# Performance work log

Measured on AMD Instinct MI355X. Metric: run time of the kernel, lower is better.

The kernel has to match this reference:

```python
import jax, jax.numpy as jnp
import numpy as np

N = 100000   # nodes
E = 1600000  # edges
H = 128      # hidden_channels
G = 2        # group
D = H // G   # per-group channels
L = 2        # num_layers
T = 112      # num_tasks
MSG_EPS = 1e-7


def _ln(x, g, b):
    mu = jnp.mean(x, axis=-1, keepdims=True)
    var = jnp.var(x, axis=-1, keepdims=True)
    return (x - mu) * jax.lax.rsqrt(var + 1e-5) * g + b


def setup_inputs() -> dict:
    key = jax.random.key(0)
    ks = jax.random.split(key, 12)
    s8, s16, sH, sD = 1/np.sqrt(8), 1/np.sqrt(16), 1/np.sqrt(H), 1/np.sqrt(D)
    inp = {}
    inp["x"] = jax.random.uniform(ks[0], (N, 8), jnp.float32)
    inp["node_index"] = jax.random.randint(ks[1], (N,), 0, N)
    inp["edge_index"] = jax.random.randint(ks[2], (2, E), 0, N)
    inp["edge_attr"] = jax.random.uniform(ks[3], (E, 8), jnp.float32)
    inp["node_features"] = jax.random.normal(ks[4], (N, 8), jnp.float32)
    inp["W_oh"] = jax.random.normal(ks[5], (8, 8)) * s8
    inp["b_oh"] = jnp.zeros((8,))
    inp["W_ne"] = jax.random.normal(ks[6], (16, H)) * s16
    inp["b_ne"] = jnp.zeros((H,))
    inp["W_ee"] = jax.random.normal(ks[7], (8, H)) * s8
    inp["b_ee"] = jnp.zeros((H,))
    inp["ln_g"] = jnp.ones((L, G, D))
    inp["ln_b"] = jnp.zeros((L, G, D))
    inp["We"] = jax.random.normal(ks[8], (L, G, H, D)) * sH   # GENConv edge encoder per Fm
    inp["be"] = jnp.zeros((L, G, D))
    inp["Wm"] = jax.random.normal(ks[9], (L, G, D, D)) * sD   # GENConv 1-layer MLP
    inp["bm"] = jnp.zeros((L, G, D))
    inp["last_g"] = jnp.ones((H,))
    inp["last_b"] = jnp.zeros((H,))
    inp["Wp"] = jax.random.normal(ks[10], (H, T)) * sH
    inp["bp"] = jnp.zeros((T,))
    return inp


def _gen_block(y_in, src, dst, ee, g, b, We_, be_, Wm_, bm_):
    # GENBlock (res+ pre-activation): norm -> relu -> GENConv(softmax aggr, t=1)
    h = jax.nn.relu(_ln(y_in, g, b))                       # [N,D]
    msg = jax.nn.relu(h[src] + ee @ We_ + be_) + MSG_EPS   # [E,D]
    mx = jax.lax.stop_gradient(jax.ops.segment_max(msg, dst, num_segments=N))
    mx = jnp.where(jnp.isfinite(mx), mx, 0.0)
    ex = jnp.exp(msg - mx[dst])
    den = jax.ops.segment_sum(ex, dst, num_segments=N)
    w = ex / (den[dst] + 1e-16)                            # scatter_softmax weights
    agg = jax.ops.segment_sum(msg * w, dst, num_segments=N)  # [N,D]
    return (h + agg) @ Wm_ + bm_


def reference(x, node_index, edge_index, edge_attr, node_features, W_oh, b_oh, W_ne, b_ne, W_ee, b_ee, ln_g, ln_b, We, be, Wm, bm, last_g, last_b, Wp, bp):
    nf1 = node_features[node_index]                        # [N,8]
    nf2 = x @ W_oh + b_oh                                  # one-hot encoder [N,8]
    h = jnp.concatenate([nf1, nf2], axis=1) @ W_ne + b_ne  # [N,H]
    ee = edge_attr @ W_ee + b_ee                           # [E,H]; cat of G copies chunks back to identical [E,H]
    src, dst = edge_index[0], edge_index[1]
    for l in range(L):
        # GroupAdditiveCoupling (group=2): y_i = x_i + F_i(y_{i-1})
        x1, x2 = jnp.split(h, G, axis=-1)
        y1 = x1 + _gen_block(x2, src, dst, ee, ln_g[l, 0], ln_b[l, 0], We[l, 0], be[l, 0], Wm[l, 0], bm[l, 0])
        y2 = x2 + _gen_block(y1, src, dst, ee, ln_g[l, 1], ln_b[l, 1], We[l, 1], be[l, 1], Wm[l, 1], bm[l, 1])
        h = jnp.concatenate([y1, y2], axis=-1)
    h = jax.nn.relu(_ln(h, last_g, last_b))
    return h @ Wp + bp
```

## Files before the change

### kernel.cpp

```cpp
#include <hip/hip_runtime.h>

constexpr int N_NODES = 100000;
constexpr int N_EDGES = 1600000;
constexpr int T_OUT = 112;

constexpr int SCAN_CHUNK = 1024;
constexpr int SCAN_BLOCKS = (N_NODES + SCAN_CHUNK - 1) / SCAN_CHUNK;

typedef _Float16 h2v __attribute__((ext_vector_type(2)));
typedef _Float16 half4 __attribute__((ext_vector_type(4)));
typedef _Float16 half8 __attribute__((ext_vector_type(8)));
typedef float f32x4 __attribute__((ext_vector_type(4)));
typedef int i4v __attribute__((ext_vector_type(4)));
typedef float f4v __attribute__((ext_vector_type(4)));

__device__ __forceinline__ float dot2h(h2v a, h2v b, float c) {
#if __has_builtin(__builtin_amdgcn_fdot2)
    return __builtin_amdgcn_fdot2(a, b, c, false);
#else
    return fmaf((float)a.x, (float)b.x, fmaf((float)a.y, (float)b.y, c));
#endif
}
__device__ __forceinline__ int pk2(float a, float b) {
    auto v = __builtin_amdgcn_cvt_pkrtz(a, b);
    return __builtin_bit_cast(int, v);
}
__device__ __forceinline__ h2v b2h(int x) { return __builtin_bit_cast(h2v, x); }
__device__ __forceinline__ unsigned short f2h(float f) {
    return __builtin_bit_cast(unsigned short, (_Float16)f);
}
__device__ __forceinline__ float h2f(unsigned short u) {
    return (float)__builtin_bit_cast(_Float16, u);
}

__global__ void wcomb_kernel(const float* __restrict__ W_ee,
                             const float* __restrict__ b_ee,
                             const float* __restrict__ We,
                             const float* __restrict__ be,
                             int* __restrict__ Wc_h2,
                             float* __restrict__ bcomb) {
    int lg = blockIdx.x;
    int d = threadIdx.x;
    const float* We_ = We + (size_t)lg * 128 * 64;
    float acc[9];
#pragma unroll
    for (int k = 0; k < 9; ++k) acc[k] = 0.f;
    for (int c = 0; c < 128; ++c) {
        float wv = We_[c * 64 + d];
#pragma unroll
        for (int k = 0; k < 8; ++k) acc[k] += W_ee[k * 128 + c] * wv;
        acc[8] += b_ee[c] * wv;
    }
#pragma unroll
    for (int j = 0; j < 4; ++j)
        Wc_h2[lg * 256 + j * 64 + d] = pk2(acc[2 * j], acc[2 * j + 1]);
    bcomb[lg * 64 + d] = acc[8] + be[lg * 64 + d];
}

__global__ void wp_pack_kernel(const float* __restrict__ Wp, int* __restrict__ wpfrag) {
    int tm = blockIdx.x;
    int tile = tm >> 2, m = tm & 3;
    int lane = threadIdx.x;
    int g = lane >> 4, r = lane & 15;
    int t = tile * 16 + r;
    int o[4];
#pragma unroll
    for (int p = 0; p < 4; ++p) {
        int j0 = 2 * p, j1 = 2 * p + 1;
        int k0 = m * 32 + (j0 >> 2) * 16 + g * 4 + (j0 & 3);
        int k1 = m * 32 + (j1 >> 2) * 16 + g * 4 + (j1 & 3);
        o[p] = pk2(Wp[k0 * 112 + t], Wp[k1 * 112 + t]);
    }
    int4 o4; o4.x = o[0]; o4.y = o[1]; o4.z = o[2]; o4.w = o[3];
    *(int4*)(wpfrag + ((size_t)tm * 64 + lane) * 4) = o4;
}

__global__ void wm_pack_kernel(const float* __restrict__ Wm, int* __restrict__ wmfrag) {
    int b = blockIdx.x;
    int lg = b >> 3, tm = b & 7;
    int tile = tm >> 1, m = tm & 1;
    int lane = threadIdx.x;
    int g = lane >> 4, r = lane & 15;
    const float* W = Wm + (size_t)lg * 4096;
    int col = tile * 16 + r;
    int o[4];
#pragma unroll
    for (int p = 0; p < 4; ++p) {
        int j0 = 2 * p, j1 = 2 * p + 1;
        int k0 = m * 32 + (j0 >> 2) * 16 + g * 4 + (j0 & 3);
        int k1 = m * 32 + (j1 >> 2) * 16 + g * 4 + (j1 & 3);
        o[p] = pk2(W[k0 * 64 + col], W[k1 * 64 + col]);
    }
    int4 o4; o4.x = o[0]; o4.y = o[1]; o4.z = o[2]; o4.w = o[3];
    *(int4*)(wmfrag + ((size_t)b * 64 + lane) * 4) = o4;
}

__global__ __launch_bounds__(256) void encoder_kernel(
    const float* __restrict__ x, const int* __restrict__ node_index,
    const float* __restrict__ node_features,
    const float* __restrict__ W_oh, const float* __restrict__ b_oh,
    const float* __restrict__ W_ne, const float* __restrict__ b_ne,
    float* __restrict__ A, float* __restrict__ B) {
    int tid = threadIdx.x;
    int w = tid >> 6, d = tid & 63;
    int n = blockIdx.x * 4 + w;

    float xf[8];
    const float* xr = x + (size_t)n * 8;
#pragma unroll
    for (int j = 0; j < 8; ++j) xf[j] = xr[j];

    float nf[16];
    int ni = node_index[n];
    const float* nfr = node_features + (size_t)ni * 8;
#pragma unroll
    for (int k = 0; k < 8; ++k) nf[k] = nfr[k];
#pragma unroll
    for (int k = 0; k < 8; ++k) {
        float acc = b_oh[k];
#pragma unroll
        for (int j = 0; j < 8; ++j) acc += xf[j] * W_oh[j * 8 + k];
        nf[8 + k] = acc;
    }
    float hA = b_ne[d], hB = b_ne[64 + d];
#pragma unroll
    for (int k = 0; k < 16; ++k) {
        hA += nf[k] * W_ne[k * 128 + d];
        hB += nf[k] * W_ne[k * 128 + 64 + d];
    }
    A[(size_t)n * 64 + d] = hA;
    B[(size_t)n * 64 + d] = hB;
}

__global__ void hist_kernel(const int* __restrict__ edge_index,
                            int* __restrict__ deg, int* __restrict__ rank) {
    int e = blockIdx.x * 256 + threadIdx.x;
    if (e < N_EDGES) rank[e] = atomicAdd(&deg[edge_index[N_EDGES + e]], 1);
}

__global__ __launch_bounds__(256) void block_sum_kernel(const int* __restrict__ deg,
                                                        int* __restrict__ blocksum) {
    __shared__ int s_w[4];
    int t = threadIdx.x;
    int base = blockIdx.x * SCAN_CHUNK + t * 4;
    int s = 0;
    if (base + 3 < N_NODES) {
        int4 v = *(const int4*)(deg + base);
        s = v.x + v.y + v.z + v.w;
    } else {
        for (int j = 0; j < 4; ++j)
            if (base + j < N_NODES) s += deg[base + j];
    }
#pragma unroll
    for (int o = 32; o >= 1; o >>= 1) s += __shfl_xor(s, o, 64);
    if ((t & 63) == 0) s_w[t >> 6] = s;
    __syncthreads();
    if (t == 0) blocksum[blockIdx.x] = s_w[0] + s_w[1] + s_w[2] + s_w[3];
}

__global__ __launch_bounds__(64) void scan_sums_kernel(const int* __restrict__ blocksum,
                                                       int* __restrict__ blockoff,
                                                       int* __restrict__ rowptr) {
    int t = threadIdx.x;
    int i0 = 2 * t, i1 = 2 * t + 1;
    int v0 = (i0 < SCAN_BLOCKS) ? blocksum[i0] : 0;
    int v1 = (i1 < SCAN_BLOCKS) ? blocksum[i1] : 0;
    int s = v0 + v1;
    int incl = s;
#pragma unroll
    for (int o = 1; o < 64; o <<= 1) {
        int u = __shfl_up(incl, o, 64);
        if (t >= o) incl += u;
    }
    int excl = incl - s;
    if (i0 < SCAN_BLOCKS) blockoff[i0] = excl;
    if (i1 < SCAN_BLOCKS) blockoff[i1] = excl + v0;
    if (t == 63) rowptr[N_NODES] = incl;
}

__global__ __launch_bounds__(256) void emit_kernel(const int* __restrict__ deg,
                                                   const int* __restrict__ blockoff,
                                                   int* __restrict__ rowptr) {
    __shared__ int s_w[4];
    int t = threadIdx.x;
    int w = t >> 6, lane = t & 63;
    int base = blockIdx.x * SCAN_CHUNK + t * 4;

    int d0 = 0, d1 = 0, d2 = 0, d3 = 0;
    if (base + 3 < N_NODES) {
        int4 v = *(const int4*)(deg + base);
        d0 = v.x; d1 = v.y; d2 = v.z; d3 = v.w;
    } else {
        if (base + 0 < N_NODES) d0 = deg[base + 0];
        if (base + 1 < N_NODES) d1 = deg[base + 1];
        if (base + 2 < N_NODES) d2 = deg[base + 2];
        if (base + 3 < N_NODES) d3 = deg[base + 3];
    }
    int s = d0 + d1 + d2 + d3;
    int incl = s;
#pragma unroll
    for (int o = 1; o < 64; o <<= 1) {
        int u = __shfl_up(incl, o, 64);
        if (lane >= o) incl += u;
    }
    if (lane == 63) s_w[w] = incl;
    __syncthreads();
    int woff = 0;
    for (int j = 0; j < 4; ++j) woff += (j < w) ? s_w[j] : 0;

    int p = blockoff[blockIdx.x] + woff + incl - s;
    int4 r;
    r.x = p;
    r.y = p + d0;
    r.z = p + d0 + d1;
    r.w = p + d0 + d1 + d2;
    if (base + 3 < N_NODES) {
        *(int4*)(rowptr + base) = r;
    } else {
        if (base + 0 < N_NODES) rowptr[base + 0] = r.x;
        if (base + 1 < N_NODES) rowptr[base + 1] = r.y;
        if (base + 2 < N_NODES) rowptr[base + 2] = r.z;
        if (base + 3 < N_NODES) rowptr[base + 3] = r.w;
    }
}

__global__ void scatter_kernel(const int* __restrict__ edge_index,
                               const float* __restrict__ edge_attr,
                               const int* __restrict__ rowptr,
                               const int* __restrict__ rank,
                               int* __restrict__ src_perm,
                               int* __restrict__ ea_h) {
    int e = blockIdx.x * 256 + threadIdx.x;
    if (e >= N_EDGES) return;
    int dn = edge_index[N_EDGES + e];
    int idx = rowptr[dn] + rank[e];
    f4v a = __builtin_nontemporal_load((const f4v*)(edge_attr + (size_t)e * 8));
    f4v b = __builtin_nontemporal_load((const f4v*)(edge_attr + (size_t)e * 8 + 4));
    i4v o;
    o.x = pk2(a.x, a.y);
    o.y = pk2(a.z, a.w);
    o.z = pk2(b.x, b.y);
    o.w = pk2(b.z, b.w);
    __builtin_nontemporal_store(o, (i4v*)(ea_h + (size_t)idx * 4));
    __builtin_nontemporal_store(edge_index[e], src_perm + idx);
}

__global__ __launch_bounds__(256) void ln_relu_kernel(const float* __restrict__ Y,
                                                      const float* __restrict__ g,
                                                      const float* __restrict__ b,
                                                      unsigned short* __restrict__ hl16) {
    int tid = threadIdx.x;
    int w = tid >> 6, d = tid & 63;
    int n = blockIdx.x * 4 + w;
    float y = Y[(size_t)n * 64 + d];
    float s = y, sq = y * y;
#pragma unroll
    for (int offd = 32; offd >= 1; offd >>= 1) {
        s += __shfl_xor(s, offd, 64);
        sq += __shfl_xor(sq, offd, 64);
    }
    float mean = s * (1.f / 64.f);
    float var = sq * (1.f / 64.f) - mean * mean;
    float rs = rsqrtf(var + 1e-5f);
    float h = (y - mean) * rs * g[d] + b[d];
    hl16[(size_t)n * 64 + d] = f2h(fmaxf(h, 0.f));
}

__global__ __launch_bounds__(256) void agg_kernel(
    const unsigned short* __restrict__ hl_in, unsigned short* __restrict__ v16,
    const int* __restrict__ rowptr, const int* __restrict__ src_perm,
    const int* __restrict__ ea_h,
    const int* __restrict__ Wc_h2, const float* __restrict__ bcomb) {
    int tid = threadIdx.x;
    int w = tid >> 6, lane = tid & 63;
    int half = lane >> 5;
    int c = (lane & 31) * 2;
    int n = blockIdx.x * 8 + w * 2 + half;

    h2v wc0[4], wc1[4];
#pragma unroll
    for (int j = 0; j < 4; ++j) {
        wc0[j] = b2h(Wc_h2[j * 64 + c]);
        wc1[j] = b2h(Wc_h2[j * 64 + c + 1]);
    }
    float bc0 = bcomb[c], bc1 = bcomb[c + 1];

    float num0 = 0.f, den0 = 0.f, num1 = 0.f, den1 = 0.f;
    int start = rowptr[n], end = rowptr[n + 1];
    const int4* ea4 = (const int4*)ea_h;

#define EDGE(U, E)                                                        \
    {                                                                     \
        h2v hv = b2h((int)(U));                                           \
        float eW0 = bc0, eW1 = bc1;                                       \
        eW0 = dot2h(b2h(E.x), wc0[0], eW0);                               \
        eW1 = dot2h(b2h(E.x), wc1[0], eW1);                               \
        eW0 = dot2h(b2h(E.y), wc0[1], eW0);                               \
        eW1 = dot2h(b2h(E.y), wc1[1], eW1);                               \
        eW0 = dot2h(b2h(E.z), wc0[2], eW0);                               \
        eW1 = dot2h(b2h(E.z), wc1[2], eW1);                               \
        eW0 = dot2h(b2h(E.w), wc0[3], eW0);                               \
        eW1 = dot2h(b2h(E.w), wc1[3], eW1);                               \
        float m0 = fmaxf((float)hv.x + eW0, 0.f) + 1e-7f;                 \
        float m1 = fmaxf((float)hv.y + eW1, 0.f) + 1e-7f;                 \
        float x0 = __expf(m0), x1 = __expf(m1);                           \
        den0 += x0; num0 += x0 * m0;                                      \
        den1 += x1; num1 += x1 * m1;                                      \
    }

    int i = start;
    for (; i + 4 <= end; i += 4) {
        int s0 = src_perm[i + 0];
        int s1 = src_perm[i + 1];
        int s2 = src_perm[i + 2];
        int s3 = src_perm[i + 3];
        unsigned int u0 = *(const unsigned int*)(hl_in + (size_t)s0 * 64 + c);
        unsigned int u1 = *(const unsigned int*)(hl_in + (size_t)s1 * 64 + c);
        unsigned int u2 = *(const unsigned int*)(hl_in + (size_t)s2 * 64 + c);
        unsigned int u3 = *(const unsigned int*)(hl_in + (size_t)s3 * 64 + c);
        int4 e0 = ea4[i + 0], e1 = ea4[i + 1], e2 = ea4[i + 2], e3 = ea4[i + 3];
        EDGE(u0, e0) EDGE(u1, e1) EDGE(u2, e2) EDGE(u3, e3)
    }
    for (; i < end; ++i) {
        int s0 = src_perm[i];
        unsigned int u0 = *(const unsigned int*)(hl_in + (size_t)s0 * 64 + c);
        int4 e0 = ea4[i];
        EDGE(u0, e0)
    }
#undef EDGE

    float agg0 = num0 / (den0 + 1e-16f);
    float agg1 = num1 / (den1 + 1e-16f);
    unsigned int uself = *(const unsigned int*)(hl_in + (size_t)n * 64 + c);
    h2v sv = b2h((int)uself);
    int vout = pk2((float)sv.x + agg0, (float)sv.y + agg1);
    *(int*)(v16 + (size_t)n * 64 + c) = vout;
}

template <bool PRODUCE_HL>
__global__ __launch_bounds__(256) void epi_kernel(
    const unsigned short* __restrict__ v16, float* __restrict__ Y,
    const int* __restrict__ wmfrag, const float* __restrict__ bm,
    const float* __restrict__ gnext, const float* __restrict__ bnext,
    unsigned short* __restrict__ hl_out) {
    int tid = threadIdx.x;
    int w = tid >> 6, lane = tid & 63;
    int g = lane >> 4, r = lane & 15;
    int nodebase = blockIdx.x * 64 + w * 16;
    if (nodebase >= N_NODES) return;

    const unsigned short* vp = v16 + (size_t)(nodebase + r) * 64;
    half8 af[2];
#pragma unroll
    for (int m = 0; m < 2; ++m) {
        int k0 = m * 32 + g * 4;
        half4 lo = *(const half4*)(vp + k0);
        half4 hi = *(const half4*)(vp + k0 + 16);
        af[m][0] = lo[0]; af[m][1] = lo[1]; af[m][2] = lo[2]; af[m][3] = lo[3];
        af[m][4] = hi[0]; af[m][5] = hi[1]; af[m][6] = hi[2]; af[m][7] = hi[3];
    }

    const int4* wf4 = (const int4*)wmfrag;
    f32x4 acc[4];
#pragma unroll
    for (int tile = 0; tile < 4; ++tile) {
        float bmv = bm[tile * 16 + r];
        acc[tile] = {bmv, bmv, bmv, bmv};
#pragma unroll
        for (int m = 0; m < 2; ++m) {
            int4 bw = wf4[(tile * 2 + m) * 64 + lane];
            half8 bf = __builtin_bit_cast(half8, bw);
            acc[tile] = __builtin_amdgcn_mfma_f32_16x16x32_f16(af[m], bf, acc[tile], 0, 0, 0);
        }
    }

    float yn[4][4];
#pragma unroll
    for (int tile = 0; tile < 4; ++tile) {
#pragma unroll
        for (int q = 0; q < 4; ++q) {
            size_t idx = (size_t)(nodebase + g * 4 + q) * 64 + tile * 16 + r;
            float y = Y[idx] + acc[tile][q];
            yn[tile][q] = y;
            Y[idx] = y;
        }
    }

    if constexpr (PRODUCE_HL) {
        float gnv[4], bnv[4];
#pragma unroll
        for (int tile = 0; tile < 4; ++tile) {
            gnv[tile] = gnext[tile * 16 + r];
            bnv[tile] = bnext[tile * 16 + r];
        }
#pragma unroll
        for (int q = 0; q < 4; ++q) {
            float s = yn[0][q] + yn[1][q] + yn[2][q] + yn[3][q];
            float sq = yn[0][q] * yn[0][q] + yn[1][q] * yn[1][q]
                     + yn[2][q] * yn[2][q] + yn[3][q] * yn[3][q];
            s += __shfl_xor(s, 1, 64);  sq += __shfl_xor(sq, 1, 64);
            s += __shfl_xor(s, 2, 64);  sq += __shfl_xor(sq, 2, 64);
            s += __shfl_xor(s, 4, 64);  sq += __shfl_xor(sq, 4, 64);
            s += __shfl_xor(s, 8, 64);  sq += __shfl_xor(sq, 8, 64);
            float mean = s * (1.f / 64.f);
            float var = sq * (1.f / 64.f) - mean * mean;
            float rs = rsqrtf(var + 1e-5f);
#pragma unroll
            for (int tile = 0; tile < 4; ++tile) {
                float h = (yn[tile][q] - mean) * rs * gnv[tile] + bnv[tile];
                hl_out[(size_t)(nodebase + g * 4 + q) * 64 + tile * 16 + r] =
                    f2h(fmaxf(h, 0.f));
            }
        }
    }
}

__global__ __launch_bounds__(256) void final_kernel(
    const float* __restrict__ A, const float* __restrict__ B,
    const float* __restrict__ lg, const float* __restrict__ lb,
    const int* __restrict__ wpfrag, const float* __restrict__ bp,
    float* __restrict__ out) {
    int tid = threadIdx.x;
    int w = tid >> 6, lane = tid & 63;
    int g = lane >> 4, r = lane & 15;
    int nodebase = blockIdx.x * 64 + w * 16;
    if (nodebase >= N_NODES) return;
    int n = nodebase + r;

    float4 v[8];
    const float4* A4 = (const float4*)(A + (size_t)n * 64);
    const float4* B4 = (const float4*)(B + (size_t)n * 64);
#pragma unroll
    for (int kb = 0; kb < 4; ++kb) v[kb] = A4[kb * 4 + g];
#pragma unroll
    for (int kb = 0; kb < 4; ++kb) v[4 + kb] = B4[kb * 4 + g];

    float s = 0.f, sq = 0.f;
#pragma unroll
    for (int kb = 0; kb < 8; ++kb) {
        s += v[kb].x + v[kb].y + v[kb].z + v[kb].w;
        sq += v[kb].x * v[kb].x + v[kb].y * v[kb].y
            + v[kb].z * v[kb].z + v[kb].w * v[kb].w;
    }
    s += __shfl_xor(s, 16, 64);  sq += __shfl_xor(sq, 16, 64);
    s += __shfl_xor(s, 32, 64);  sq += __shfl_xor(sq, 32, 64);
    float mean = s * (1.f / 128.f);
    float var = sq * (1.f / 128.f) - mean * mean;
    float rs = rsqrtf(var + 1e-5f);

    const float4* lg4 = (const float4*)lg;
    const float4* lb4 = (const float4*)lb;
    half8 afr[4];
#pragma unroll
    for (int kb = 0; kb < 8; ++kb) {
        float4 gv = lg4[kb * 4 + g];
        float4 bv = lb4[kb * 4 + g];
        int m = kb >> 1, e0 = (kb & 1) * 4;
        afr[m][e0 + 0] = (_Float16)fmaxf((v[kb].x - mean) * rs * gv.x + bv.x, 0.f);
        afr[m][e0 + 1] = (_Float16)fmaxf((v[kb].y - mean) * rs * gv.y + bv.y, 0.f);
        afr[m][e0 + 2] = (_Float16)fmaxf((v[kb].z - mean) * rs * gv.z + bv.z, 0.f);
        afr[m][e0 + 3] = (_Float16)fmaxf((v[kb].w - mean) * rs * gv.w + bv.w, 0.f);
    }

    const int4* wf4 = (const int4*)wpfrag;
#pragma unroll
    for (int tile = 0; tile < 7; ++tile) {
        float bias = bp[tile * 16 + r];
        f32x4 acc = {bias, bias, bias, bias};
#pragma unroll
        for (int m = 0; m < 4; ++m) {
            int4 bw = wf4[(tile * 4 + m) * 64 + lane];
            half8 bf = __builtin_bit_cast(half8, bw);
            acc = __builtin_amdgcn_mfma_f32_16x16x32_f16(afr[m], bf, acc, 0, 0, 0);
        }
#pragma unroll
        for (int q = 0; q < 4; ++q) {
            out[(size_t)(nodebase + g * 4 + q) * T_OUT + tile * 16 + r] = acc[q];
        }
    }
}

extern "C" void kernel_launch(void* const* d_in, const int* in_sizes, int n_in,
                              void* d_out, int out_size, void* d_ws, size_t ws_size,
                              hipStream_t stream) {
    const float* x            = (const float*)d_in[0];
    const int* node_index     = (const int*)d_in[1];
    const int* edge_index     = (const int*)d_in[2];
    const float* edge_attr    = (const float*)d_in[3];
    const float* node_features= (const float*)d_in[4];
    const float* W_oh         = (const float*)d_in[5];
    const float* b_oh         = (const float*)d_in[6];
    const float* W_ne         = (const float*)d_in[7];
    const float* b_ne         = (const float*)d_in[8];
    const float* W_ee         = (const float*)d_in[9];
    const float* b_ee         = (const float*)d_in[10];
    const float* ln_g         = (const float*)d_in[11];
    const float* ln_b         = (const float*)d_in[12];
    const float* We           = (const float*)d_in[13];
    const float* be           = (const float*)d_in[14];
    const float* Wm           = (const float*)d_in[15];
    const float* bm           = (const float*)d_in[16];
    const float* last_g       = (const float*)d_in[17];
    const float* last_b       = (const float*)d_in[18];
    const float* Wp           = (const float*)d_in[19];
    const float* bp           = (const float*)d_in[20];
    float* out = (float*)d_out;

    char* ws = (char*)d_ws;
    size_t off = 0;
    auto alloc = [&](size_t bytes) -> void* {
        void* p = ws + off;
        off = (off + bytes + 255) & ~(size_t)255;
        return p;
    };
    float* A          = (float*)alloc((size_t)N_NODES * 64 * 4);
    float* B          = (float*)alloc((size_t)N_NODES * 64 * 4);
    unsigned short* hl = (unsigned short*)alloc((size_t)N_NODES * 64 * 2);
    unsigned short* v16 = (unsigned short*)alloc((size_t)N_NODES * 64 * 2);
    int* deg          = (int*)alloc((size_t)N_NODES * 4);
    int* rowptr       = (int*)alloc((size_t)(N_NODES + 1) * 4);
    int* rank         = (int*)alloc((size_t)N_EDGES * 4);
    int* src_perm     = (int*)alloc((size_t)N_EDGES * 4);
    int* ea_h         = (int*)alloc((size_t)N_EDGES * 4 * 4);
    int* Wc_h2        = (int*)alloc(4 * 256 * 4);
    float* bcomb      = (float*)alloc(4 * 64 * 4);
    int* blocksum     = (int*)alloc((size_t)SCAN_BLOCKS * 4);
    int* blockoff     = (int*)alloc((size_t)SCAN_BLOCKS * 4);
    int* wpfrag       = (int*)alloc((size_t)28 * 64 * 16);
    int* wmfrag       = (int*)alloc((size_t)32 * 64 * 16);
    (void)ws_size; (void)in_sizes; (void)n_in; (void)out_size;

    const int NB_NODE = N_NODES / 4;
    const int NB_EDGE = (N_EDGES + 255) / 256;
    const int NB_AGG  = N_NODES / 8;
    const int NB_EPI  = (N_NODES + 63) / 64;

    (void)hipMemsetAsync(deg, 0, (size_t)N_NODES * 4, stream);
    wcomb_kernel<<<4, 64, 0, stream>>>(W_ee, b_ee, We, be, Wc_h2, bcomb);
    wp_pack_kernel<<<28, 64, 0, stream>>>(Wp, wpfrag);
    wm_pack_kernel<<<32, 64, 0, stream>>>(Wm, wmfrag);
    encoder_kernel<<<NB_NODE, 256, 0, stream>>>(x, node_index, node_features,
                                                W_oh, b_oh, W_ne, b_ne, A, B);
    hist_kernel<<<NB_EDGE, 256, 0, stream>>>(edge_index, deg, rank);
    block_sum_kernel<<<SCAN_BLOCKS, 256, 0, stream>>>(deg, blocksum);
    scan_sums_kernel<<<1, 64, 0, stream>>>(blocksum, blockoff, rowptr);
    emit_kernel<<<SCAN_BLOCKS, 256, 0, stream>>>(deg, blockoff, rowptr);
    scatter_kernel<<<NB_EDGE, 256, 0, stream>>>(edge_index, edge_attr, rowptr,
                                                rank, src_perm, ea_h);

    ln_relu_kernel<<<NB_NODE, 256, 0, stream>>>(B, ln_g, ln_b, hl);

    agg_kernel<<<NB_AGG, 256, 0, stream>>>(hl, v16, rowptr, src_perm, ea_h,
                                           Wc_h2 + 0 * 256, bcomb + 0 * 64);
    epi_kernel<true><<<NB_EPI, 256, 0, stream>>>(
        v16, A, wmfrag + 0 * 8 * 256, bm + 0 * 64,
        ln_g + 1 * 64, ln_b + 1 * 64, hl);
    agg_kernel<<<NB_AGG, 256, 0, stream>>>(hl, v16, rowptr, src_perm, ea_h,
                                           Wc_h2 + 1 * 256, bcomb + 1 * 64);
    epi_kernel<true><<<NB_EPI, 256, 0, stream>>>(
        v16, B, wmfrag + 1 * 8 * 256, bm + 1 * 64,
        ln_g + 2 * 64, ln_b + 2 * 64, hl);
    agg_kernel<<<NB_AGG, 256, 0, stream>>>(hl, v16, rowptr, src_perm, ea_h,
                                           Wc_h2 + 2 * 256, bcomb + 2 * 64);
    epi_kernel<true><<<NB_EPI, 256, 0, stream>>>(
        v16, A, wmfrag + 2 * 8 * 256, bm + 2 * 64,
        ln_g + 3 * 64, ln_b + 3 * 64, hl);
    agg_kernel<<<NB_AGG, 256, 0, stream>>>(hl, v16, rowptr, src_perm, ea_h,
                                           Wc_h2 + 3 * 256, bcomb + 3 * 64);
    epi_kernel<false><<<NB_EPI, 256, 0, stream>>>(
        v16, B, wmfrag + 3 * 8 * 256, bm + 3 * 64,
        nullptr, nullptr, nullptr);

    final_kernel<<<NB_EPI, 256, 0, stream>>>(A, B, last_g, last_b, wpfrag, bp, out);
}
```

Baseline: 608.0 us.

## Two-pass bucketed edge scatter and switch node features from fp16 to fp32

```diff
diff --git a/kernel.cpp b/kernel.cpp
--- a/kernel.cpp
+++ b/kernel.cpp
@@ -7,11 +7,14 @@
 constexpr int SCAN_CHUNK = 1024;
 constexpr int SCAN_BLOCKS = (N_NODES + SCAN_CHUNK - 1) / SCAN_CHUNK;
 
+constexpr int BKT_SHIFT = 9;
+constexpr int NBKT = (N_NODES + 511) / 512;
+constexpr int CHUNK = 4096;
+constexpr int NCHUNK = (N_EDGES + CHUNK - 1) / CHUNK;
+
 typedef _Float16 h2v __attribute__((ext_vector_type(2)));
-typedef _Float16 half4 __attribute__((ext_vector_type(4)));
 typedef _Float16 half8 __attribute__((ext_vector_type(8)));
 typedef float f32x4 __attribute__((ext_vector_type(4)));
-typedef int i4v __attribute__((ext_vector_type(4)));
 typedef float f4v __attribute__((ext_vector_type(4)));
 
 __device__ __forceinline__ float dot2h(h2v a, h2v b, float c) {
@@ -26,12 +29,6 @@
     return __builtin_bit_cast(int, v);
 }
 __device__ __forceinline__ h2v b2h(int x) { return __builtin_bit_cast(h2v, x); }
-__device__ __forceinline__ unsigned short f2h(float f) {
-    return __builtin_bit_cast(unsigned short, (_Float16)f);
-}
-__device__ __forceinline__ float h2f(unsigned short u) {
-    return (float)__builtin_bit_cast(_Float16, u);
-}
 
 __global__ void wcomb_kernel(const float* __restrict__ W_ee,
                              const float* __restrict__ b_ee,
@@ -132,10 +129,25 @@
     B[(size_t)n * 64 + d] = hB;
 }
 
-__global__ void hist_kernel(const int* __restrict__ edge_index,
-                            int* __restrict__ deg, int* __restrict__ rank) {
-    int e = blockIdx.x * 256 + threadIdx.x;
-    if (e < N_EDGES) rank[e] = atomicAdd(&deg[edge_index[N_EDGES + e]], 1);
+__global__ __launch_bounds__(256) void hist_count_kernel(
+    const int* __restrict__ edge_index, int* __restrict__ deg,
+    int* __restrict__ rank, int* __restrict__ C) {
+    __shared__ int lcnt[NBKT];
+    int tid = threadIdx.x;
+    int chunk = blockIdx.x;
+    if (tid < NBKT) lcnt[tid] = 0;
+    __syncthreads();
+#pragma unroll
+    for (int it = 0; it < CHUNK / 256; ++it) {
+        int e = chunk * CHUNK + it * 256 + tid;
+        if (e < N_EDGES) {
+            int dn = edge_index[N_EDGES + e];
+            rank[e] = atomicAdd(&deg[dn], 1);
+            atomicAdd(&lcnt[dn >> BKT_SHIFT], 1);
+        }
+    }
+    __syncthreads();
+    if (tid < NBKT) C[chunk * NBKT + tid] = lcnt[tid];
 }
 
 __global__ __launch_bounds__(256) void block_sum_kernel(const int* __restrict__ deg,
@@ -224,31 +236,112 @@
     }
 }
 
-__global__ void scatter_kernel(const int* __restrict__ edge_index,
-                               const float* __restrict__ edge_attr,
-                               const int* __restrict__ rowptr,
-                               const int* __restrict__ rank,
-                               int* __restrict__ src_perm,
-                               int* __restrict__ ea_h) {
-    int e = blockIdx.x * 256 + threadIdx.x;
-    if (e >= N_EDGES) return;
-    int dn = edge_index[N_EDGES + e];
-    int idx = rowptr[dn] + rank[e];
-    f4v a = __builtin_nontemporal_load((const f4v*)(edge_attr + (size_t)e * 8));
-    f4v b = __builtin_nontemporal_load((const f4v*)(edge_attr + (size_t)e * 8 + 4));
-    i4v o;
-    o.x = pk2(a.x, a.y);
-    o.y = pk2(a.z, a.w);
-    o.z = pk2(b.x, b.y);
-    o.w = pk2(b.z, b.w);
-    __builtin_nontemporal_store(o, (i4v*)(ea_h + (size_t)idx * 4));
-    __builtin_nontemporal_store(edge_index[e], src_perm + idx);
+__global__ __launch_bounds__(64) void col_total_kernel(const int* __restrict__ C,
+                                                       int* __restrict__ total) {
+    int b = blockIdx.x, t = threadIdx.x;
+    int s = 0;
+    for (int c = t; c < NCHUNK; c += 64) s += C[c * NBKT + b];
+#pragma unroll
+    for (int o = 32; o >= 1; o >>= 1) s += __shfl_xor(s, o, 64);
+    if (t == 0) total[b] = s;
+}
+
+__global__ __launch_bounds__(64) void base_scan_kernel(const int* __restrict__ total,
+                                                       int* __restrict__ base) {
+    int t = threadIdx.x;
+    int v[4];
+    int s = 0;
+#pragma unroll
+    for (int j = 0; j < 4; ++j) {
+        int i = t * 4 + j;
+        v[j] = (i < NBKT) ? total[i] : 0;
+        s += v[j];
+    }
+    int incl = s;
+#pragma unroll
+    for (int o = 1; o < 64; o <<= 1) {
+        int u = __shfl_up(incl, o, 64);
+        if (t >= o) incl += u;
+    }
+    int prefix = incl - s;
+#pragma unroll
+    for (int j = 0; j < 4; ++j) {
+        int i = t * 4 + j;
+        if (i < NBKT) base[i] = prefix;
+        prefix += v[j];
+    }
+    if (t == 63) base[NBKT] = incl;
+}
+
+__global__ __launch_bounds__(64) void chunk_off_kernel(const int* __restrict__ C,
+                                                       const int* __restrict__ base,
+                                                       int* __restrict__ OFF) {
+    int b = blockIdx.x, t = threadIdx.x;
+    int running = base[b];
+    for (int g = 0; g * 64 < NCHUNK; ++g) {
+        int c = g * 64 + t;
+        int v = (c < NCHUNK) ? C[c * NBKT + b] : 0;
+        int incl = v;
+#pragma unroll
+        for (int o = 1; o < 64; o <<= 1) {
+            int u = __shfl_up(incl, o, 64);
+            if (t >= o) incl += u;
+        }
+        if (c < NCHUNK) OFF[c * NBKT + b] = running + incl - v;
+        running += __shfl(incl, 63, 64);
+    }
+}
+
+__global__ __launch_bounds__(256) void partition_kernel(
+    const int* __restrict__ edge_index, const float* __restrict__ edge_attr,
+    const int* __restrict__ rowptr, const int* __restrict__ rank,
+    const int* __restrict__ OFF,
+    int4* __restrict__ st_ea, int* __restrict__ st_src, int* __restrict__ st_idx) {
+    __shared__ int cur[NBKT];
+    int tid = threadIdx.x;
+    int chunk = blockIdx.x;
+    if (tid < NBKT) cur[tid] = OFF[chunk * NBKT + tid];
+    __syncthreads();
+#pragma unroll
+    for (int it = 0; it < CHUNK / 256; ++it) {
+        int e = chunk * CHUNK + it * 256 + tid;
+        if (e < N_EDGES) {
+            int dn = edge_index[N_EDGES + e];
+            int b = dn >> BKT_SHIFT;
+            int p = atomicAdd(&cur[b], 1);
+            f4v a = __builtin_nontemporal_load((const f4v*)(edge_attr + (size_t)e * 8));
+            f4v bb = __builtin_nontemporal_load((const f4v*)(edge_attr + (size_t)e * 8 + 4));
+            int4 o;
+            o.x = pk2(a.x, a.y);
+            o.y = pk2(a.z, a.w);
+            o.z = pk2(bb.x, bb.y);
+            o.w = pk2(bb.z, bb.w);
+            st_ea[p] = o;
+            st_src[p] = edge_index[e];
+            st_idx[p] = rowptr[dn] + rank[e];
+        }
+    }
+}
+
+__global__ __launch_bounds__(512) void place_kernel(
+    const int* __restrict__ base,
+    const int4* __restrict__ st_ea, const int* __restrict__ st_src,
+    const int* __restrict__ st_idx,
+    int* __restrict__ src_perm, int* __restrict__ ea_h) {
+    int b = blockIdx.x;
+    int s = base[b], e_end = base[b + 1];
+    for (int i = s + threadIdx.x; i < e_end; i += 512) {
+        int4 v = st_ea[i];
+        int idx = st_idx[i];
+        *(int4*)(ea_h + (size_t)idx * 4) = v;
+        src_perm[idx] = st_src[i];
+    }
 }
 
 __global__ __launch_bounds__(256) void ln_relu_kernel(const float* __restrict__ Y,
                                                       const float* __restrict__ g,
                                                       const float* __restrict__ b,
-                                                      unsigned short* __restrict__ hl16) {
+                                                      float* __restrict__ hl) {
     int tid = threadIdx.x;
     int w = tid >> 6, d = tid & 63;
     int n = blockIdx.x * 4 + w;
@@ -263,11 +356,11 @@
     float var = sq * (1.f / 64.f) - mean * mean;
     float rs = rsqrtf(var + 1e-5f);
     float h = (y - mean) * rs * g[d] + b[d];
-    hl16[(size_t)n * 64 + d] = f2h(fmaxf(h, 0.f));
+    hl[(size_t)n * 64 + d] = fmaxf(h, 0.f);
 }
 
 __global__ __launch_bounds__(256) void agg_kernel(
-    const unsigned short* __restrict__ hl_in, unsigned short* __restrict__ v16,
+    const float* __restrict__ hl_in, float* __restrict__ v32,
     const int* __restrict__ rowptr, const int* __restrict__ src_perm,
     const int* __restrict__ ea_h,
     const int* __restrict__ Wc_h2, const float* __restrict__ bcomb) {
@@ -291,7 +384,6 @@
 
 #define EDGE(U, E)                                                        \
     {                                                                     \
-        h2v hv = b2h((int)(U));                                           \
         float eW0 = bc0, eW1 = bc1;                                       \
         eW0 = dot2h(b2h(E.x), wc0[0], eW0);                               \
         eW1 = dot2h(b2h(E.x), wc1[0], eW1);                               \
@@ -301,8 +393,8 @@
         eW1 = dot2h(b2h(E.z), wc1[2], eW1);                               \
         eW0 = dot2h(b2h(E.w), wc0[3], eW0);                               \
         eW1 = dot2h(b2h(E.w), wc1[3], eW1);                               \
-        float m0 = fmaxf((float)hv.x + eW0, 0.f) + 1e-7f;                 \
-        float m1 = fmaxf((float)hv.y + eW1, 0.f) + 1e-7f;                 \
+        float m0 = fmaxf(U.x + eW0, 0.f) + 1e-7f;                         \
+        float m1 = fmaxf(U.y + eW1, 0.f) + 1e-7f;                         \
         float x0 = __expf(m0), x1 = __expf(m1);                           \
         den0 += x0; num0 += x0 * m0;                                      \
         den1 += x1; num1 += x1 * m1;                                      \
@@ -314,16 +406,16 @@
         int s1 = src_perm[i + 1];
         int s2 = src_perm[i + 2];
         int s3 = src_perm[i + 3];
-        unsigned int u0 = *(const unsigned int*)(hl_in + (size_t)s0 * 64 + c);
-        unsigned int u1 = *(const unsigned int*)(hl_in + (size_t)s1 * 64 + c);
-        unsigned int u2 = *(const unsigned int*)(hl_in + (size_t)s2 * 64 + c);
-        unsigned int u3 = *(const unsigned int*)(hl_in + (size_t)s3 * 64 + c);
+        float2 u0 = *(const float2*)(hl_in + (size_t)s0 * 64 + c);
+        float2 u1 = *(const float2*)(hl_in + (size_t)s1 * 64 + c);
+        float2 u2 = *(const float2*)(hl_in + (size_t)s2 * 64 + c);
+        float2 u3 = *(const float2*)(hl_in + (size_t)s3 * 64 + c);
         int4 e0 = ea4[i + 0], e1 = ea4[i + 1], e2 = ea4[i + 2], e3 = ea4[i + 3];
         EDGE(u0, e0) EDGE(u1, e1) EDGE(u2, e2) EDGE(u3, e3)
     }
     for (; i < end; ++i) {
         int s0 = src_perm[i];
-        unsigned int u0 = *(const unsigned int*)(hl_in + (size_t)s0 * 64 + c);
+        float2 u0 = *(const float2*)(hl_in + (size_t)s0 * 64 + c);
         int4 e0 = ea4[i];
         EDGE(u0, e0)
     }
@@ -331,33 +423,36 @@
 
     float agg0 = num0 / (den0 + 1e-16f);
     float agg1 = num1 / (den1 + 1e-16f);
-    unsigned int uself = *(const unsigned int*)(hl_in + (size_t)n * 64 + c);
-    h2v sv = b2h((int)uself);
-    int vout = pk2((float)sv.x + agg0, (float)sv.y + agg1);
-    *(int*)(v16 + (size_t)n * 64 + c) = vout;
+    float2 sv = *(const float2*)(hl_in + (size_t)n * 64 + c);
+    float2 vout;
+    vout.x = sv.x + agg0;
+    vout.y = sv.y + agg1;
+    *(float2*)(v32 + (size_t)n * 64 + c) = vout;
 }
 
 template <bool PRODUCE_HL>
 __global__ __launch_bounds__(256) void epi_kernel(
-    const unsigned short* __restrict__ v16, float* __restrict__ Y,
+    const float* __restrict__ v32, float* __restrict__ Y,
     const int* __restrict__ wmfrag, const float* __restrict__ bm,
     const float* __restrict__ gnext, const float* __restrict__ bnext,
-    unsigned short* __restrict__ hl_out) {
+    float* __restrict__ hl_out) {
     int tid = threadIdx.x;
     int w = tid >> 6, lane = tid & 63;
     int g = lane >> 4, r = lane & 15;
     int nodebase = blockIdx.x * 64 + w * 16;
     if (nodebase >= N_NODES) return;
 
-    const unsigned short* vp = v16 + (size_t)(nodebase + r) * 64;
+    const float* vp = v32 + (size_t)(nodebase + r) * 64;
     half8 af[2];
 #pragma unroll
     for (int m = 0; m < 2; ++m) {
         int k0 = m * 32 + g * 4;
-        half4 lo = *(const half4*)(vp + k0);
-        half4 hi = *(const half4*)(vp + k0 + 16);
-        af[m][0] = lo[0]; af[m][1] = lo[1]; af[m][2] = lo[2]; af[m][3] = lo[3];
-        af[m][4] = hi[0]; af[m][5] = hi[1]; af[m][6] = hi[2]; af[m][7] = hi[3];
+        float4 lo = *(const float4*)(vp + k0);
+        float4 hi = *(const float4*)(vp + k0 + 16);
+        af[m][0] = (_Float16)lo.x; af[m][1] = (_Float16)lo.y;
+        af[m][2] = (_Float16)lo.z; af[m][3] = (_Float16)lo.w;
+        af[m][4] = (_Float16)hi.x; af[m][5] = (_Float16)hi.y;
+        af[m][6] = (_Float16)hi.z; af[m][7] = (_Float16)hi.w;
     }
 
     const int4* wf4 = (const int4*)wmfrag;
@@ -409,7 +504,7 @@
             for (int tile = 0; tile < 4; ++tile) {
                 float h = (yn[tile][q] - mean) * rs * gnv[tile] + bnv[tile];
                 hl_out[(size_t)(nodebase + g * 4 + q) * 64 + tile * 16 + r] =
-                    f2h(fmaxf(h, 0.f));
+                    fmaxf(h, 0.f);
             }
         }
     }
@@ -515,8 +610,8 @@
     };
     float* A          = (float*)alloc((size_t)N_NODES * 64 * 4);
     float* B          = (float*)alloc((size_t)N_NODES * 64 * 4);
-    unsigned short* hl = (unsigned short*)alloc((size_t)N_NODES * 64 * 2);
-    unsigned short* v16 = (unsigned short*)alloc((size_t)N_NODES * 64 * 2);
+    float* hl         = (float*)alloc((size_t)N_NODES * 64 * 4);
+    float* v32        = (float*)alloc((size_t)N_NODES * 64 * 4);
     int* deg          = (int*)alloc((size_t)N_NODES * 4);
     int* rowptr       = (int*)alloc((size_t)(N_NODES + 1) * 4);
     int* rank         = (int*)alloc((size_t)N_EDGES * 4);
@@ -528,10 +623,16 @@
     int* blockoff     = (int*)alloc((size_t)SCAN_BLOCKS * 4);
     int* wpfrag       = (int*)alloc((size_t)28 * 64 * 16);
     int* wmfrag       = (int*)alloc((size_t)32 * 64 * 16);
+    int* Cmat         = (int*)alloc((size_t)NCHUNK * NBKT * 4);
+    int* OFFmat       = (int*)alloc((size_t)NCHUNK * NBKT * 4);
+    int* btotal       = (int*)alloc(256 * 4);
+    int* bbase        = (int*)alloc(256 * 4);
+    int* st_src       = (int*)d_out;
+    int* st_idx       = (int*)d_out + N_EDGES;
+    int4* st_ea       = (int4*)((int*)d_out + 2 * (size_t)N_EDGES);
     (void)ws_size; (void)in_sizes; (void)n_in; (void)out_size;
 
     const int NB_NODE = N_NODES / 4;
-    const int NB_EDGE = (N_EDGES + 255) / 256;
     const int NB_AGG  = N_NODES / 8;
     const int NB_EPI  = (N_NODES + 63) / 64;
 
@@ -541,34 +642,39 @@
     wm_pack_kernel<<<32, 64, 0, stream>>>(Wm, wmfrag);
     encoder_kernel<<<NB_NODE, 256, 0, stream>>>(x, node_index, node_features,
                                                 W_oh, b_oh, W_ne, b_ne, A, B);
-    hist_kernel<<<NB_EDGE, 256, 0, stream>>>(edge_index, deg, rank);
+    hist_count_kernel<<<NCHUNK, 256, 0, stream>>>(edge_index, deg, rank, Cmat);
     block_sum_kernel<<<SCAN_BLOCKS, 256, 0, stream>>>(deg, blocksum);
     scan_sums_kernel<<<1, 64, 0, stream>>>(blocksum, blockoff, rowptr);
     emit_kernel<<<SCAN_BLOCKS, 256, 0, stream>>>(deg, blockoff, rowptr);
-    scatter_kernel<<<NB_EDGE, 256, 0, stream>>>(edge_index, edge_attr, rowptr,
-                                                rank, src_perm, ea_h);
+    col_total_kernel<<<NBKT, 64, 0, stream>>>(Cmat, btotal);
+    base_scan_kernel<<<1, 64, 0, stream>>>(btotal, bbase);
+    chunk_off_kernel<<<NBKT, 64, 0, stream>>>(Cmat, bbase, OFFmat);
+    partition_kernel<<<NCHUNK, 256, 0, stream>>>(edge_index, edge_attr, rowptr,
+                                                 rank, OFFmat, st_ea, st_src, st_idx);
+    place_kernel<<<NBKT, 512, 0, stream>>>(bbase, st_ea, st_src, st_idx,
+                                           src_perm, ea_h);
 
     ln_relu_kernel<<<NB_NODE, 256, 0, stream>>>(B, ln_g, ln_b, hl);
 
-    agg_kernel<<<NB_AGG, 256, 0, stream>>>(hl, v16, rowptr, src_perm, ea_h,
+    agg_kernel<<<NB_AGG, 256, 0, stream>>>(hl, v32, rowptr, src_perm, ea_h,
                                            Wc_h2 + 0 * 256, bcomb + 0 * 64);
     epi_kernel<true><<<NB_EPI, 256, 0, stream>>>(
-        v16, A, wmfrag + 0 * 8 * 256, bm + 0 * 64,
+        v32, A, wmfrag + 0 * 8 * 256, bm + 0 * 64,
         ln_g + 1 * 64, ln_b + 1 * 64, hl);
-    agg_kernel<<<NB_AGG, 256, 0, stream>>>(hl, v16, rowptr, src_perm, ea_h,
+    agg_kernel<<<NB_AGG, 256, 0, stream>>>(hl, v32, rowptr, src_perm, ea_h,
                                            Wc_h2 + 1 * 256, bcomb + 1 * 64);
     epi_kernel<true><<<NB_EPI, 256, 0, stream>>>(
-        v16, B, wmfrag + 1 * 8 * 256, bm + 1 * 64,
+        v32, B, wmfrag + 1 * 8 * 256, bm + 1 * 64,
         ln_g + 2 * 64, ln_b + 2 * 64, hl);
-    agg_kernel<<<NB_AGG, 256, 0, stream>>>(hl, v16, rowptr, src_perm, ea_h,
+    agg_kernel<<<NB_AGG, 256, 0, stream>>>(hl, v32, rowptr, src_perm, ea_h,
                                            Wc_h2 + 2 * 256, bcomb + 2 * 64);
     epi_kernel<true><<<NB_EPI, 256, 0, stream>>>(
-        v16, A, wmfrag + 2 * 8 * 256, bm + 2 * 64,
+        v32, A, wmfrag + 2 * 8 * 256, bm + 2 * 64,
         ln_g + 3 * 64, ln_b + 3 * 64, hl);
-    agg_kernel<<<NB_AGG, 256, 0, stream>>>(hl, v16, rowptr, src_perm, ea_h,
+    agg_kernel<<<NB_AGG, 256, 0, stream>>>(hl, v32, rowptr, src_perm, ea_h,
                                            Wc_h2 + 3 * 256, bcomb + 3 * 64);
     epi_kernel<false><<<NB_EPI, 256, 0, stream>>>(
-        v16, B, wmfrag + 3 * 8 * 256, bm + 3 * 64,
+        v32, B, wmfrag + 3 * 8 * 256, bm + 3 * 64,
         nullptr, nullptr, nullptr);
 
     final_kernel<<<NB_EPI, 256, 0, stream>>>(A, B, last_g, last_b, wpfrag, bp, out);
```

After: 692.9 us. +14.0%, slower.
